# Kernel tuning notes

Hardware: AMD Instinct MI355X
Metric: run time of the kernel (lower is better)

The kernel has to match this reference:

```python
import jax, jax.numpy as jnp
import numpy as np

B, T, E, H, V, K = 32, 256, 256, 256, 32000, 48
PAD = 0


def setup_inputs() -> dict:
    key = jax.random.key(0)
    ks = jax.random.split(key, 24)
    lengths = jnp.sort(jax.random.randint(ks[0], (B,), 1, T + 1))[::-1]
    lengths = lengths.at[0].set(T)  # pack_padded needs max length present
    sent = jax.random.randint(ks[1], (B, T), 1, V)
    pos = jnp.arange(T)[None, :]
    sentence = jnp.where(pos < lengths[:, None], sent, PAD)
    tags = jax.random.randint(ks[2], (B, T), 0, K)
    s = 0.1
    p = {"sentence": sentence, "lengths": lengths, "tags": tags}
    p["embed"] = jax.random.normal(ks[3], (V, E)) * s
    dims = [E, 2 * H]
    i = 4
    for l in range(2):
        for d in ("f", "b"):
            p[f"Wih_{l}{d}"] = jax.random.normal(ks[i], (4 * H, dims[l])) * s; i += 1
            p[f"Whh_{l}{d}"] = jax.random.normal(ks[i], (4 * H, H)) * s; i += 1
            p[f"b_{l}{d}"] = jax.random.normal(ks[i], (4 * H,)) * s; i += 1
    p["Wout"] = jax.random.normal(ks[i], (K, 2 * H)) * s; i += 1
    p["bout"] = jax.random.normal(ks[i], (K,)) * s; i += 1
    p["start_t"] = jax.random.normal(ks[i], (K,)) * s; i += 1
    p["end_t"] = jax.random.normal(ks[i], (K,)) * s; i += 1
    p["trans"] = jax.random.normal(ks[i], (K, K)) * s
    return p


def _lstm_dir(x, m, Wih, Whh, b, reverse):
    # x: [T,B,D] time-major, m: [T,B] bool. Masked update emulates pack_padded_sequence.
    if reverse:
        x, m = x[::-1], m[::-1]
    Bn, Hn = x.shape[1], Whh.shape[1]

    def step(carry, inp):
        h, c = carry
        xt, mt = inp
        g = xt @ Wih.T + h @ Whh.T + b
        i_, f_, g_, o_ = jnp.split(g, 4, axis=-1)
        c2 = jax.nn.sigmoid(f_) * c + jax.nn.sigmoid(i_) * jnp.tanh(g_)
        h2 = jax.nn.sigmoid(o_) * jnp.tanh(c2)
        mm = mt[:, None]
        h2 = jnp.where(mm, h2, h)
        c2 = jnp.where(mm, c2, c)
        return (h2, c2), jnp.where(mm, h2, 0.0)

    init = (jnp.zeros((Bn, Hn), x.dtype), jnp.zeros((Bn, Hn), x.dtype))
    _, hs = jax.lax.scan(step, init, (x, m))
    return hs[::-1] if reverse else hs


def _forward(sentence, tags, embed, layer_params, Wout, bout, start_t, end_t, trans):
    mask = sentence != PAD                      # [B,T]
    x = embed[sentence]                          # [B,T,E]
    xt = jnp.transpose(x, (1, 0, 2))             # [T,B,E]
    mt = mask.T                                  # [T,B]
    for (Wf, Uf, bf, Wb, Ub, bb) in layer_params:
        hf = _lstm_dir(xt, mt, Wf, Uf, bf, False)
        hb = _lstm_dir(xt, mt, Wb, Ub, bb, True)
        xt = jnp.concatenate([hf, hb], axis=-1)  # [T,B,2H]
    emit = xt @ Wout.T + bout                    # [T,B,K]; dropout is identity in eval

    # ---- CRF log-likelihood (torchcrf) ----
    mf = mt.astype(emit.dtype)
    tt = tags.T                                  # [T,B]
    bar = jnp.arange(sentence.shape[0])
    num = start_t[tt[0]] + emit[0, bar, tt[0]]

    def num_step(s, inp):
        em, tg, pg, m = inp
        return s + (trans[pg, tg] + em[bar, tg]) * m, None

    num, _ = jax.lax.scan(num_step, num, (emit[1:], tt[1:], tt[:-1], mf[1:]))
    last_idx = mf.sum(0).astype(jnp.int32) - 1
    last_tags = tt[last_idx, bar]
    num = num + end_t[last_tags]

    score = start_t[None, :] + emit[0]           # [B,K]

    def den_step(s, inp):
        em, m = inp
        nxt = jax.nn.logsumexp(s[:, :, None] + trans[None] + em[:, None, :], axis=1)
        return jnp.where(m[:, None] > 0, nxt, s), None

    score, _ = jax.lax.scan(den_step, score, (emit[1:], mf[1:]))
    den = jax.nn.logsumexp(score + end_t[None, :], axis=1)
    loss = (num - den).mean()                    # torchcrf reduction='mean' log-likelihood
    return jnp.transpose(emit, (1, 0, 2)), loss, mask


def reference(sentence, lengths, tags, embed,
              Wih_0f, Whh_0f, b_0f, Wih_0b, Whh_0b, b_0b,
              Wih_1f, Whh_1f, b_1f, Wih_1b, Whh_1b, b_1b,
              Wout, bout, start_t, end_t, trans):
    layers = [(Wih_0f, Whh_0f, b_0f, Wih_0b, Whh_0b, b_0b),
              (Wih_1f, Whh_1f, b_1f, Wih_1b, Whh_1b, b_1b)]
    return _forward(sentence, tags, embed, layers, Wout, bout, start_t, end_t, trans)
```

## Files before the change

kernel.cpp:

```cpp
#include <hip/hip_runtime.h>

#define Bz 32
#define Tz 256
#define Ez 256
#define Hz 256
#define Kz 48
#define G4 1024
#define H2 512

typedef __attribute__((ext_vector_type(8))) short short8;
typedef __attribute__((ext_vector_type(4))) float f32x4;
typedef unsigned short ushort_t;
typedef unsigned int uint_t;
typedef unsigned long long ull_t;

__device__ __forceinline__ float bf2f(ushort_t u) {
    unsigned int x = ((unsigned int)u) << 16;
    union { unsigned int i; float f; } c; c.i = x; return c.f;
}
__device__ __forceinline__ ushort_t f2bf(float f) {
    union { float f; unsigned int i; } c; c.f = f;
    unsigned int x = c.i;
    unsigned int lsb = (x >> 16) & 1u;
    x += 0x7fffu + lsb;
    return (ushort_t)(x >> 16);
}
__device__ __forceinline__ float sigm(float x) { return 1.f / (1.f + __expf(-x)); }
__device__ __forceinline__ float tanh_f(float x) { return 1.f - 2.f / (__expf(2.f * x) + 1.f); }

#define MFMA16(a, b, c) __builtin_amdgcn_mfma_f32_16x16x32_bf16((a), (b), (c), 0, 0, 0)

struct CvtArgs {
    const float* s[9];
    ushort_t* d[9];
    int n[9];
};
__global__ __launch_bounds__(256) void cvt_all(CvtArgs a)
{
    int y = blockIdx.y;
    const float* src = a.s[y];
    ushort_t* dst = a.d[y];
    int n = a.n[y];
    int i = (blockIdx.x * 256 + threadIdx.x) * 4;
    if (i < n) {
        float4 v = *(const float4*)(src + i);
        ushort_t o[4] = { f2bf(v.x), f2bf(v.y), f2bf(v.z), f2bf(v.w) };
        *(uint2*)(dst + i) = *(uint2*)o;
    }
}

__global__ __launch_bounds__(64) void embed_kernel(
    const int* __restrict__ sent, const float* __restrict__ embed,
    ushort_t* __restrict__ emb, float* __restrict__ mask_out)
{
    int blk = blockIdx.x;
    int b = blk >> 8, t = blk & 255;
    int s = sent[blk];
    int tid = threadIdx.x;
    float4 v = *(const float4*)(embed + (size_t)s * Ez + tid * 4);
    ushort_t o[4] = { f2bf(v.x), f2bf(v.y), f2bf(v.z), f2bf(v.w) };
    *(uint2*)(emb + ((size_t)t * Bz + b) * Ez + tid * 4) = *(uint2*)o;
    if (tid == 0) mask_out[blk] = (s != 0) ? 1.0f : 0.0f;
}

__global__ __launch_bounds__(256) void gemm_xproj(
    const ushort_t* __restrict__ A,
    const ushort_t* __restrict__ Wf, const ushort_t* __restrict__ Wb,
    const float* __restrict__ biasf, const float* __restrict__ biasb,
    ushort_t* __restrict__ Cf, ushort_t* __restrict__ Cb,
    int M, int Kd)
{
    const ushort_t* W = blockIdx.z ? Wb : Wf;
    const float* bias = blockIdx.z ? biasb : biasf;
    ushort_t* C = blockIdx.z ? Cb : Cf;
    int m0 = blockIdx.x * 64, n0 = blockIdx.y * 64;
    int tid = threadIdx.x, l = tid & 63, w = tid >> 6;
    int mw = m0 + (w & 1) * 32, nw = n0 + (w >> 1) * 32;
    int lr = l & 15, lq = l >> 4;
    f32x4 acc[2][2] = {};
    for (int ko = 0; ko < Kd; ko += 32) {
        short8 a0 = *(const short8*)(A + (size_t)(mw + lr) * Kd + ko + lq * 8);
        short8 a1 = *(const short8*)(A + (size_t)(mw + 16 + lr) * Kd + ko + lq * 8);
        short8 b0 = *(const short8*)(W + (size_t)(nw + lr) * Kd + ko + lq * 8);
        short8 b1 = *(const short8*)(W + (size_t)(nw + 16 + lr) * Kd + ko + lq * 8);
        acc[0][0] = MFMA16(a0, b0, acc[0][0]);
        acc[0][1] = MFMA16(a0, b1, acc[0][1]);
        acc[1][0] = MFMA16(a1, b0, acc[1][0]);
        acc[1][1] = MFMA16(a1, b1, acc[1][1]);
    }
    for (int mt = 0; mt < 2; mt++)
        for (int nt = 0; nt < 2; nt++)
            for (int r = 0; r < 4; r++) {
                int row = mw + mt * 16 + lq * 4 + r;
                int col = nw + nt * 16 + lr;
                float v = acc[mt][nt][r] + bias[col];
                C[(size_t)row * G4 + col] = f2bf(v);
            }
}

#define LDK 264

__global__ __launch_bounds__(256, 1) void lstm_layer(
    const ushort_t* __restrict__ Whh_f, const ushort_t* __restrict__ Whh_b,
    const ushort_t* __restrict__ Xp_f, const ushort_t* __restrict__ Xp_b,
    const int* __restrict__ lengths,
    ushort_t* __restrict__ hcat,
    ull_t* __restrict__ hbuf)
{
    __shared__ __attribute__((aligned(16))) ushort_t sH[Bz][LDK];
    __shared__ float sG[4][16][34];

    int bid = blockIdx.x;
    int dir = bid >> 4;
    int sub = bid & 15;
    int h0 = sub * 16;
    const ushort_t* Whh = dir ? Whh_b : Whh_f;
    const ushort_t* Xp  = dir ? Xp_b  : Xp_f;
    int tid = threadIdx.x, l = tid & 63, w = tid >> 6;
    int lr = l & 15, lq = l >> 4;
    int mw = (w & 1) * 16;
    int P  = w >> 1;
    int U0w = h0 + P * 8;

    short8 bw0[8], bw1[8];
    int gA = (lr & 3) * Hz + U0w + (lr >> 2);
    int gB = gA + 4;
    {
        const ushort_t* W0 = Whh + (size_t)gA * Hz;
        const ushort_t* W1 = Whh + (size_t)gB * Hz;
        #pragma unroll
        for (int k = 0; k < 8; k++) {
            bw0[k] = *(const short8*)(W0 + k * 32 + lq * 8);
            bw1[k] = *(const short8*)(W1 + k * 32 + lq * 8);
        }
    }

    int upd = (l < 32);
    int bloc = l & 15;
    int q = (l >> 4) & 1;
    int batch = mw + bloc;
    int lenb = lengths[batch];
    float c4[4] = {0.f, 0.f, 0.f, 0.f};
    ull_t prevw = 0;
    int pubw = batch * 64 + sub * 4 + P * 2 + q;
    int hcoff = dir * Hz + U0w + q * 4;

    for (int s = 0; s < Tz; s++) {
        int t_act = dir ? (Tz - 1 - s) : s;
        const ushort_t* Xrow = Xp + (size_t)t_act * Bz * G4;

        float xv0[4], xv1[4];
        #pragma unroll
        for (int r = 0; r < 4; r++) {
            int brow = mw + lq * 4 + r;
            xv0[r] = bf2f(Xrow[(size_t)brow * G4 + gA]);
            xv1[r] = bf2f(Xrow[(size_t)brow * G4 + gB]);
        }

        const ull_t* hcur = hbuf + ((s & 1) * 2 + dir) * (Bz * Hz / 4);
        uint_t tagc = (uint_t)(((s >> 1) ^ s) & 1);
        ull_t vals[8];
        uint_t pend = 0xffu;
        while (pend) {
            #pragma unroll
            for (int k = 0; k < 8; k++)
                if (pend & (1u << k))
                    vals[k] = __hip_atomic_load(&hcur[k * 256 + tid],
                                                __ATOMIC_RELAXED, __HIP_MEMORY_SCOPE_AGENT);
            #pragma unroll
            for (int k = 0; k < 8; k++)
                if ((pend & (1u << k)) && (((uint_t)(vals[k] >> 14) & 1u) == tagc))
                    pend &= ~(1u << k);
        }
        #pragma unroll
        for (int k = 0; k < 8; k++) {
            int idx = k * 256 + tid;
            *(ull_t*)(&sH[idx >> 6][(idx & 63) * 4]) = vals[k] & ~(1ull << 14);
        }
        __syncthreads();

        f32x4 acc0 = {}, acc1 = {};
        #pragma unroll
        for (int k = 0; k < 8; k++) {
            short8 a = *(const short8*)(&sH[mw + lr][k * 32 + lq * 8]);
            acc0 = MFMA16(a, bw0[k], acc0);
            acc1 = MFMA16(a, bw1[k], acc1);
        }
        #pragma unroll
        for (int r = 0; r < 4; r++) {
            sG[w][lq * 4 + r][lr]      = acc0[r] + xv0[r];
            sG[w][lq * 4 + r][16 + lr] = acc1[r] + xv1[r];
        }
        asm volatile("s_waitcnt lgkmcnt(0)" ::: "memory");

        uint_t tagp = (uint_t)((((s + 1) >> 1) ^ (s + 1)) & 1);
        if (upd) {
            int msk = (t_act < lenb);
            ushort_t hx[4], hc[4];
            const ushort_t* ho = (const ushort_t*)&prevw;
            #pragma unroll
            for (int j = 0; j < 4; j++) {
                int cb = q * 16 + j * 4;
                float gi = sG[w][bloc][cb], gf = sG[w][bloc][cb + 1];
                float gg = sG[w][bloc][cb + 2], go = sG[w][bloc][cb + 3];
                float c2 = sigm(gf) * c4[j] + sigm(gi) * tanh_f(gg);
                float h2 = sigm(go) * tanh_f(c2);
                if (msk) c4[j] = c2;
                ushort_t hn = f2bf(h2);
                hx[j] = msk ? hn : ho[j];
                hc[j] = msk ? hn : (ushort_t)0;
            }
            ull_t wd; __builtin_memcpy(&wd, hx, 8);
            prevw = wd;
            wd |= ((ull_t)tagp) << 14;
            ull_t* hnxt = hbuf + (((s + 1) & 1) * 2 + dir) * (Bz * Hz / 4);
            __hip_atomic_store(&hnxt[pubw], wd,
                               __ATOMIC_RELAXED, __HIP_MEMORY_SCOPE_AGENT);
            ull_t wc; __builtin_memcpy(&wc, hc, 8);
            *(ull_t*)(hcat + ((size_t)t_act * Bz + batch) * H2 + hcoff) = wc;
        }
    }
}

__global__ __launch_bounds__(256) void gemm_emit(
    const ushort_t* __restrict__ A, const ushort_t* __restrict__ Wout,
    const float* __restrict__ bout, float* __restrict__ emit_out)
{
    int tid = threadIdx.x, l = tid & 63, w = tid >> 6;
    int m0 = blockIdx.x * 64 + w * 16;
    int lr = l & 15, lq = l >> 4;
    f32x4 acc[3] = {};
    for (int ko = 0; ko < H2; ko += 32) {
        short8 a = *(const short8*)(A + (size_t)(m0 + lr) * H2 + ko + lq * 8);
        #pragma unroll
        for (int nt = 0; nt < 3; nt++) {
            short8 bfr = *(const short8*)(Wout + (size_t)(nt * 16 + lr) * H2 + ko + lq * 8);
            acc[nt] = MFMA16(a, bfr, acc[nt]);
        }
    }
    #pragma unroll
    for (int nt = 0; nt < 3; nt++)
        #pragma unroll
        for (int r = 0; r < 4; r++) {
            int row = m0 + lq * 4 + r;
            int col = nt * 16 + lr;
            float v = acc[nt][r] + bout[col];
            int t = row >> 5, b = row & 31;
            emit_out[((size_t)b * Tz + t) * Kz + col] = v;
        }
}

__global__ __launch_bounds__(256) void crf_num(
    const float* __restrict__ emit, const int* __restrict__ sent,
    const int* __restrict__ tags, const int* __restrict__ lengths,
    const float* __restrict__ trans, const float* __restrict__ start_t,
    const float* __restrict__ end_t, float* __restrict__ num)
{
    __shared__ float red[4];
    int b = blockIdx.x, t = threadIdx.x;
    int tg = tags[b * Tz + t];
    float term;
    if (t == 0) {
        term = start_t[tg] + emit[(size_t)b * Tz * Kz + tg];
        int len = lengths[b];
        term += end_t[tags[b * Tz + len - 1]];
    } else if (sent[b * Tz + t] != 0) {
        int tp = tags[b * Tz + t - 1];
        term = trans[tp * Kz + tg] + emit[((size_t)b * Tz + t) * Kz + tg];
    } else term = 0.f;
    #pragma unroll
    for (int off = 1; off < 64; off <<= 1) term += __shfl_xor(term, off);
    int w = t >> 6;
    if ((t & 63) == 0) red[w] = term;
    __syncthreads();
    if (t == 0) num[b] = red[0] + red[1] + red[2] + red[3];
}

__global__ __launch_bounds__(64) void crf_den(
    const float* __restrict__ emit, const int* __restrict__ lengths,
    const float* __restrict__ trans, const float* __restrict__ start_t,
    const float* __restrict__ end_t, float* __restrict__ den)
{
    __shared__ float sT[Kz * Kz];
    __shared__ float sS[Kz];
    int b = blockIdx.x, l = threadIdx.x;
    for (int i = l; i < Kz * Kz; i += 64) sT[i] = trans[i];
    int len = lengths[b];
    bool act = l < Kz;
    float s = act ? (start_t[l] + emit[(size_t)b * Tz * Kz + l]) : -1e30f;
    for (int t = 1; t < len; t++) {
        float em = act ? emit[((size_t)b * Tz + t) * Kz + l] : 0.f;
        if (act) sS[l] = s;
        float M = s;
        #pragma unroll
        for (int off = 1; off < 64; off <<= 1) M = fmaxf(M, __shfl_xor(M, off));
        float a0 = 0.f, a1 = 0.f, a2 = 0.f, a3 = 0.f;
        #pragma unroll 4
        for (int i = 0; i < Kz; i += 4) {
            a0 += __expf(sS[i]     + sT[i * Kz + l]       - M);
            a1 += __expf(sS[i + 1] + sT[(i + 1) * Kz + l] - M);
            a2 += __expf(sS[i + 2] + sT[(i + 2) * Kz + l] - M);
            a3 += __expf(sS[i + 3] + sT[(i + 3) * Kz + l] - M);
        }
        float sum = (a0 + a1) + (a2 + a3);
        if (act) s = em + M + __logf(sum);
    }
    float v = act ? (s + end_t[l]) : -1e30f;
    float M = v;
    #pragma unroll
    for (int off = 1; off < 64; off <<= 1) M = fmaxf(M, __shfl_xor(M, off));
    float accv = act ? __expf(v - M) : 0.f;
    #pragma unroll
    for (int off = 1; off < 64; off <<= 1) accv += __shfl_xor(accv, off);
    if (l == 0) den[b] = M + __logf(accv);
}

__global__ __launch_bounds__(64) void crf_loss(
    const float* __restrict__ num, const float* __restrict__ den, float* __restrict__ out)
{
    int l = threadIdx.x;
    float v = (l < Bz) ? (num[l] - den[l]) : 0.f;
    #pragma unroll
    for (int off = 1; off < 64; off <<= 1) v += __shfl_xor(v, off);
    if (l == 0) out[0] = v / (float)Bz;
}

extern "C" void kernel_launch(void* const* d_in, const int* in_sizes, int n_in,
                              void* d_out, int out_size, void* d_ws, size_t ws_size,
                              hipStream_t stream) {
    const int* sent      = (const int*)d_in[0];
    const int* lengths   = (const int*)d_in[1];
    const int* tags      = (const int*)d_in[2];
    const float* embed   = (const float*)d_in[3];
    const float* Wih0f = (const float*)d_in[4];
    const float* Whh0f = (const float*)d_in[5];
    const float* b0f   = (const float*)d_in[6];
    const float* Wih0b = (const float*)d_in[7];
    const float* Whh0b = (const float*)d_in[8];
    const float* b0b   = (const float*)d_in[9];
    const float* Wih1f = (const float*)d_in[10];
    const float* Whh1f = (const float*)d_in[11];
    const float* b1f   = (const float*)d_in[12];
    const float* Wih1b = (const float*)d_in[13];
    const float* Whh1b = (const float*)d_in[14];
    const float* b1b   = (const float*)d_in[15];
    const float* Wout  = (const float*)d_in[16];
    const float* bout  = (const float*)d_in[17];
    const float* start_t = (const float*)d_in[18];
    const float* end_t   = (const float*)d_in[19];
    const float* trans   = (const float*)d_in[20];

    char* ws = (char*)d_ws;
    ushort_t* Xp_f  = (ushort_t*)(ws);
    ushort_t* Xp_b  = (ushort_t*)(ws + 16777216);
    ushort_t* hcat  = (ushort_t*)(ws + 33554432);
    ushort_t* emb   = (ushort_t*)(ws + 41943040);
    ushort_t* Whh0f_c = (ushort_t*)(ws + 46137344);
    ushort_t* Whh0b_c = (ushort_t*)(ws + 46661632);
    ushort_t* Wih0f_c = (ushort_t*)(ws + 47185920);
    ushort_t* Wih0b_c = (ushort_t*)(ws + 47710208);
    ushort_t* Wih1f_c = (ushort_t*)(ws + 48234496);
    ushort_t* Wih1b_c = (ushort_t*)(ws + 49283072);
    ushort_t* Whh1f_c = (ushort_t*)(ws + 50331648);
    ushort_t* Whh1b_c = (ushort_t*)(ws + 50855936);
    ushort_t* Wout_c  = (ushort_t*)(ws + 51380224);
    ull_t*    hbufL0 = (ull_t*)(ws + 51429376);
    ull_t*    hbufL1 = (ull_t*)(ws + 51560448);
    float*    num   = (float*)   (ws + 51691520);
    float*    den   = (float*)   (ws + 51691776);

    float* out      = (float*)d_out;
    float* loss_out = out + (size_t)Bz * Tz * Kz;
    float* mask_out = loss_out + 1;

    hipMemsetAsync(hbufL0, 0, 262144, stream);

    CvtArgs ca;
    ca.s[0] = Whh0f; ca.d[0] = Whh0f_c; ca.n[0] = 262144;
    ca.s[1] = Whh0b; ca.d[1] = Whh0b_c; ca.n[1] = 262144;
    ca.s[2] = Wih0f; ca.d[2] = Wih0f_c; ca.n[2] = 262144;
    ca.s[3] = Wih0b; ca.d[3] = Wih0b_c; ca.n[3] = 262144;
    ca.s[4] = Wih1f; ca.d[4] = Wih1f_c; ca.n[4] = 524288;
    ca.s[5] = Wih1b; ca.d[5] = Wih1b_c; ca.n[5] = 524288;
    ca.s[6] = Whh1f; ca.d[6] = Whh1f_c; ca.n[6] = 262144;
    ca.s[7] = Whh1b; ca.d[7] = Whh1b_c; ca.n[7] = 262144;
    ca.s[8] = Wout;  ca.d[8] = Wout_c;  ca.n[8] = 24576;
    cvt_all<<<dim3(512, 9), 256, 0, stream>>>(ca);

    embed_kernel<<<Bz * Tz, 64, 0, stream>>>(sent, embed, emb, mask_out);

    gemm_xproj<<<dim3(Tz * Bz / 64, G4 / 64, 2), 256, 0, stream>>>(
        emb, Wih0f_c, Wih0b_c, b0f, b0b, Xp_f, Xp_b, Tz * Bz, Ez);

    lstm_layer<<<32, 256, 0, stream>>>(Whh0f_c, Whh0b_c, Xp_f, Xp_b, lengths, hcat, hbufL0);

    gemm_xproj<<<dim3(Tz * Bz / 64, G4 / 64, 2), 256, 0, stream>>>(
        hcat, Wih1f_c, Wih1b_c, b1f, b1b, Xp_f, Xp_b, Tz * Bz, H2);

    lstm_layer<<<32, 256, 0, stream>>>(Whh1f_c, Whh1b_c, Xp_f, Xp_b, lengths, hcat, hbufL1);

    gemm_emit<<<Tz * Bz / 64, 256, 0, stream>>>(hcat, Wout_c, bout, out);

    crf_num<<<Bz, 256, 0, stream>>>(out, sent, tags, lengths, trans, start_t, end_t, num);
    crf_den<<<Bz, 64, 0, stream>>>(out, lengths, trans, start_t, end_t, den);
    crf_loss<<<1, 64, 0, stream>>>(num, den, loss_out);
}
```

Baseline: 2.006 ms.

## Poll hidden-state fragments directly into MFMA operands, dropping shared-memory staging

Each wave now polls the exact 16-byte h fragments it needs for its MFMA A operand with inline-asm dwordx4 loads (sc1), checking the tag bits per fragment, instead of cooperatively loading the whole h vector into LDS and then doing a __syncthreads. This removes the LDS round trip and the block-wide barrier from the serial recurrence's critical path. In exchange, each wave redundantly loads its own h rows, and the inline asm bypasses the compiler's memory-model handling.

```diff
diff --git a/kernel.cpp b/kernel.cpp
--- a/kernel.cpp
+++ b/kernel.cpp
@@ -13,6 +13,7 @@
 typedef unsigned short ushort_t;
 typedef unsigned int uint_t;
 typedef unsigned long long ull_t;
+typedef __attribute__((ext_vector_type(4))) uint_t uint4_t;
 
 __device__ __forceinline__ float bf2f(ushort_t u) {
     unsigned int x = ((unsigned int)u) << 16;
@@ -29,6 +30,24 @@
 __device__ __forceinline__ float tanh_f(float x) { return 1.f - 2.f / (__expf(2.f * x) + 1.f); }
 
 #define MFMA16(a, b, c) __builtin_amdgcn_mfma_f32_16x16x32_bf16((a), (b), (c), 0, 0, 0)
+
+__device__ __forceinline__ void pollfrag8(const void* p, uint4_t* o)
+{
+    asm volatile(
+        "global_load_dwordx4 %0, %8, off sc1\n\t"
+        "global_load_dwordx4 %1, %8, off offset:64 sc1\n\t"
+        "global_load_dwordx4 %2, %8, off offset:128 sc1\n\t"
+        "global_load_dwordx4 %3, %8, off offset:192 sc1\n\t"
+        "global_load_dwordx4 %4, %8, off offset:256 sc1\n\t"
+        "global_load_dwordx4 %5, %8, off offset:320 sc1\n\t"
+        "global_load_dwordx4 %6, %8, off offset:384 sc1\n\t"
+        "global_load_dwordx4 %7, %8, off offset:448 sc1\n\t"
+        "s_waitcnt vmcnt(0)"
+        : "=&v"(o[0]), "=&v"(o[1]), "=&v"(o[2]), "=&v"(o[3]),
+          "=&v"(o[4]), "=&v"(o[5]), "=&v"(o[6]), "=&v"(o[7])
+        : "v"(p)
+        : "memory");
+}
 
 struct CvtArgs {
     const float* s[9];
@@ -98,7 +117,7 @@
             }
 }
 
-#define LDK 264
+#define HWRD 2048
 
 __global__ __launch_bounds__(256, 1) void lstm_layer(
     const ushort_t* __restrict__ Whh_f, const ushort_t* __restrict__ Whh_b,
@@ -107,7 +126,6 @@
     ushort_t* __restrict__ hcat,
     ull_t* __restrict__ hbuf)
 {
-    __shared__ __attribute__((aligned(16))) ushort_t sH[Bz][LDK];
     __shared__ float sG[4][16][34];
 
     int bid = blockIdx.x;
@@ -144,6 +162,7 @@
     ull_t prevw = 0;
     int pubw = batch * 64 + sub * 4 + P * 2 + q;
     int hcoff = dir * Hz + U0w + q * 4;
+    int fwoff = (mw + lr) * 64 + lq * 2;
 
     for (int s = 0; s < Tz; s++) {
         int t_act = dir ? (Tz - 1 - s) : s;
@@ -157,32 +176,29 @@
             xv1[r] = bf2f(Xrow[(size_t)brow * G4 + gB]);
         }
 
-        const ull_t* hcur = hbuf + ((s & 1) * 2 + dir) * (Bz * Hz / 4);
+        const ull_t* base = hbuf + ((s & 1) * 2 + dir) * HWRD;
+        const void* fp = (const void*)(base + fwoff);
         uint_t tagc = (uint_t)(((s >> 1) ^ s) & 1);
-        ull_t vals[8];
-        uint_t pend = 0xffu;
-        while (pend) {
+        uint4_t fr[8];
+        uint_t done = 0;
+        while (done != 0xffu) {
+            uint4_t t8[8];
+            pollfrag8(fp, t8);
             #pragma unroll
-            for (int k = 0; k < 8; k++)
-                if (pend & (1u << k))
-                    vals[k] = __hip_atomic_load(&hcur[k * 256 + tid],
-                                                __ATOMIC_RELAXED, __HIP_MEMORY_SCOPE_AGENT);
-            #pragma unroll
-            for (int k = 0; k < 8; k++)
-                if ((pend & (1u << k)) && (((uint_t)(vals[k] >> 14) & 1u) == tagc))
-                    pend &= ~(1u << k);
-        }
+            for (int k = 0; k < 8; k++) {
+                uint_t ok = (((t8[k].x >> 14) & 1u) == tagc) &
+                            (((t8[k].z >> 14) & 1u) == tagc);
+                if (!(done & (1u << k)) && ok) { fr[k] = t8[k]; done |= (1u << k); }
+            }
+        }
+        #pragma unroll
+        for (int k = 0; k < 8; k++) { fr[k].x &= ~0x4000u; fr[k].z &= ~0x4000u; }
+
+        f32x4 acc0 = {}, acc1 = {};
         #pragma unroll
         for (int k = 0; k < 8; k++) {
-            int idx = k * 256 + tid;
-            *(ull_t*)(&sH[idx >> 6][(idx & 63) * 4]) = vals[k] & ~(1ull << 14);
-        }
-        __syncthreads();
-
-        f32x4 acc0 = {}, acc1 = {};
-        #pragma unroll
-        for (int k = 0; k < 8; k++) {
-            short8 a = *(const short8*)(&sH[mw + lr][k * 32 + lq * 8]);
+            short8 a;
+            __builtin_memcpy(&a, &fr[k], 16);
             acc0 = MFMA16(a, bw0[k], acc0);
             acc1 = MFMA16(a, bw1[k], acc1);
         }
@@ -213,7 +229,7 @@
             ull_t wd; __builtin_memcpy(&wd, hx, 8);
             prevw = wd;
             wd |= ((ull_t)tagp) << 14;
-            ull_t* hnxt = hbuf + (((s + 1) & 1) * 2 + dir) * (Bz * Hz / 4);
+            ull_t* hnxt = hbuf + (((s + 1) & 1) * 2 + dir) * HWRD;
             __hip_atomic_store(&hnxt[pubw], wd,
                                __ATOMIC_RELAXED, __HIP_MEMORY_SCOPE_AGENT);
             ull_t wc; __builtin_memcpy(&wc, hc, 8);
```

Measured after the change: 2.587 ms. 1.29x slower.

## Stage xproj GEMM tiles in LDS with 128x128 blocks and direct global-to-LDS loads

Applied to the files above, without the earlier changes.

The input-projection GEMM moves from 64x64 block tiles that read operands straight from global memory to 128x128 tiles. Each k-step stages A and W into shared memory with global_load_lds, and each wave then computes a 4x4 grid of MFMA tiles. This raises operand reuse and cuts redundant global traffic. It adds two barriers per k-step with no double buffering, so loads and MFMAs do not overlap, and it launches fewer blocks.

```diff
diff --git a/kernel.cpp b/kernel.cpp
--- a/kernel.cpp
+++ b/kernel.cpp
@@ -73,26 +73,59 @@
     const ushort_t* W = blockIdx.z ? Wb : Wf;
     const float* bias = blockIdx.z ? biasb : biasf;
     ushort_t* C = blockIdx.z ? Cb : Cf;
-    int m0 = blockIdx.x * 64, n0 = blockIdx.y * 64;
+    __shared__ __attribute__((aligned(16))) ushort_t sA[128 * 32];
+    __shared__ __attribute__((aligned(16))) ushort_t sB[128 * 32];
+
+    int m0 = blockIdx.x * 128, n0 = blockIdx.y * 128;
     int tid = threadIdx.x, l = tid & 63, w = tid >> 6;
-    int mw = m0 + (w & 1) * 32, nw = n0 + (w >> 1) * 32;
     int lr = l & 15, lq = l >> 4;
-    f32x4 acc[2][2] = {};
+    int mw = (w & 1) * 64, nw = (w >> 1) * 64;
+
+    int srow_lane = l >> 2;
+    int scol_lane = (l & 3) * 8;
+
+    f32x4 acc[4][4] = {};
     for (int ko = 0; ko < Kd; ko += 32) {
-        short8 a0 = *(const short8*)(A + (size_t)(mw + lr) * Kd + ko + lq * 8);
-        short8 a1 = *(const short8*)(A + (size_t)(mw + 16 + lr) * Kd + ko + lq * 8);
-        short8 b0 = *(const short8*)(W + (size_t)(nw + lr) * Kd + ko + lq * 8);
-        short8 b1 = *(const short8*)(W + (size_t)(nw + 16 + lr) * Kd + ko + lq * 8);
-        acc[0][0] = MFMA16(a0, b0, acc[0][0]);
-        acc[0][1] = MFMA16(a0, b1, acc[0][1]);
-        acc[1][0] = MFMA16(a1, b0, acc[1][0]);
-        acc[1][1] = MFMA16(a1, b1, acc[1][1]);
-    }
-    for (int mt = 0; mt < 2; mt++)
-        for (int nt = 0; nt < 2; nt++)
+        #pragma unroll
+        for (int j = 0; j < 4; j++) {
+            int seg = w * 4 + j;
+            const ushort_t* src;
+            ushort_t* dst;
+            if (seg < 8) {
+                src = A + (size_t)(m0 + seg * 16 + srow_lane) * Kd + ko + scol_lane;
+                dst = sA + seg * 512;
+            } else {
+                src = W + (size_t)(n0 + (seg - 8) * 16 + srow_lane) * Kd + ko + scol_lane;
+                dst = sB + (seg - 8) * 512;
+            }
+            __builtin_amdgcn_global_load_lds(src, dst, 16, 0, 0);
+        }
+        asm volatile("s_waitcnt vmcnt(0)" ::: "memory");
+        __syncthreads();
+
+        short8 af[4], bf_[4];
+        #pragma unroll
+        for (int mt = 0; mt < 4; mt++)
+            af[mt] = *(const short8*)(&sA[(mw + mt * 16 + lr) * 32 + lq * 8]);
+        #pragma unroll
+        for (int nt = 0; nt < 4; nt++)
+            bf_[nt] = *(const short8*)(&sB[(nw + nt * 16 + lr) * 32 + lq * 8]);
+        #pragma unroll
+        for (int mt = 0; mt < 4; mt++)
+            #pragma unroll
+            for (int nt = 0; nt < 4; nt++)
+                acc[mt][nt] = MFMA16(af[mt], bf_[nt], acc[mt][nt]);
+        __syncthreads();
+    }
+
+    #pragma unroll
+    for (int mt = 0; mt < 4; mt++)
+        #pragma unroll
+        for (int nt = 0; nt < 4; nt++)
+            #pragma unroll
             for (int r = 0; r < 4; r++) {
-                int row = mw + mt * 16 + lq * 4 + r;
-                int col = nw + nt * 16 + lr;
+                int row = m0 + mw + mt * 16 + lq * 4 + r;
+                int col = n0 + nw + nt * 16 + lr;
                 float v = acc[mt][nt][r] + bias[col];
                 C[(size_t)row * G4 + col] = f2bf(v);
             }
@@ -389,12 +422,12 @@
 
     embed_kernel<<<Bz * Tz, 64, 0, stream>>>(sent, embed, emb, mask_out);
 
-    gemm_xproj<<<dim3(Tz * Bz / 64, G4 / 64, 2), 256, 0, stream>>>(
+    gemm_xproj<<<dim3(Tz * Bz / 128, G4 / 128, 2), 256, 0, stream>>>(
         emb, Wih0f_c, Wih0b_c, b0f, b0b, Xp_f, Xp_b, Tz * Bz, Ez);
 
     lstm_layer<<<32, 256, 0, stream>>>(Whh0f_c, Whh0b_c, Xp_f, Xp_b, lengths, hcat, hbufL0);
 
-    gemm_xproj<<<dim3(Tz * Bz / 64, G4 / 64, 2), 256, 0, stream>>>(
+    gemm_xproj<<<dim3(Tz * Bz / 128, G4 / 128, 2), 256, 0, stream>>>(
         hcat, Wih1f_c, Wih1b_c, b1f, b1b, Xp_f, Xp_b, Tz * Bz, H2);
 
     lstm_layer<<<32, 256, 0, stream>>>(Whh1f_c, Whh1b_c, Xp_f, Xp_b, lengths, hcat, hbufL1);
```

New measurement: 1.877 ms. 6.4% less time.
